# Optimization experiments

Hardware: AMD Instinct MI355X
Metric: run time of the kernel (lower is better)

Reference implementation:

```python
import jax, jax.numpy as jnp
import numpy as np

CHUNK = 128
EPS = 1e-12


def causal_prod(q, k, v, chunk=CHUNK):
    """Chunk-parallel causal linear attention numerator and denominator.
    q,k: [B,H,S,D]; v: [B,H,S,E].
    Returns N: [B,H,S,E] = q_n . cumsum_{m<=n}(k_m v_m^T)
            D: [B,H,S]   = q_n . cumsum_{m<=n} k_m
    """
    B, H, S, D = q.shape
    E = v.shape[-1]
    nc = S // chunk
    # [nc, B, H, C, D]
    qc = q.reshape(B, H, nc, chunk, D).transpose(2, 0, 1, 3, 4)
    kc = k.reshape(B, H, nc, chunk, D).transpose(2, 0, 1, 3, 4)
    vc = v.reshape(B, H, nc, chunk, E).transpose(2, 0, 1, 3, 4)
    mask = jnp.tril(jnp.ones((chunk, chunk), dtype=bool))  # j <= i

    def step(carry, xs):
        S_state, Z_state = carry  # [B,H,D,E], [B,H,D]
        qb, kb, vb = xs           # [B,H,C,D], [B,H,C,D], [B,H,C,E]
        scores = jnp.einsum('bhid,bhjd->bhij', qb, kb)
        scores = jnp.where(mask, scores, 0.0)
        # intra-chunk causal part + inter-chunk state part
        Nb = jnp.einsum('bhij,bhje->bhie', scores, vb) \
             + jnp.einsum('bhid,bhde->bhie', qb, S_state)
        Db = scores.sum(-1) + jnp.einsum('bhid,bhd->bhi', qb, Z_state)
        S_state = S_state + jnp.einsum('bhjd,bhje->bhde', kb, vb)
        Z_state = Z_state + kb.sum(axis=2)
        return (S_state, Z_state), (Nb, Db)

    init = (jnp.zeros((B, H, D, E), q.dtype), jnp.zeros((B, H, D), q.dtype))
    _, (N, Dv) = jax.lax.scan(step, init, (qc, kc, vc))
    N = N.transpose(1, 2, 0, 3, 4).reshape(B, H, S, E)
    Dv = Dv.transpose(1, 2, 0, 3).reshape(B, H, S)
    return N, Dv


def setup_inputs() -> dict:
    key = jax.random.key(0)
    k0, k1, k2, k3, k4 = jax.random.split(key, 5)
    B, H, S, D = 2, 8, 4096, 64
    # feature-mapped q/k are positive (softmax random features) -> uniform
    q = jax.random.uniform(k0, (B, H, S, D), dtype=jnp.float32)
    k = jax.random.uniform(k1, (B, H, S, D), dtype=jnp.float32)
    q_rot = jax.random.uniform(k2, (B, H, S, D), dtype=jnp.float32)
    k_rot = jax.random.uniform(k3, (B, H, S, D), dtype=jnp.float32)
    v = jax.random.normal(k4, (B, H, S, D), dtype=jnp.float32)
    return {"q": q, "k": k, "q_rot": q_rot, "k_rot": k_rot, "v": v, "horizon": 512}


def reference(q, k, q_rot, k_rot, v, horizon):
    # causal_linear_attention with local=horizon, rotary branch active
    N1, D1 = causal_prod(q, k, v)
    N2, D2 = causal_prod(q_rot, k_rot, v)
    N = N1 + N2
    Dd = D1 + D2
    local = horizon
    # subtract contribution of keys older than the local window
    ql = q[:, :, local:]
    kl = k[:, :, :-local]
    vl = v[:, :, :-local]
    qrl = q_rot[:, :, local:]
    krl = k_rot[:, :, :-local]
    Ns1, Ds1 = causal_prod(ql, kl, vl)
    Ns2, Ds2 = causal_prod(qrl, krl, vl)
    N = N.at[:, :, local:].add(-(Ns1 + Ns2))
    Dd = Dd.at[:, :, local:].add(-(Ds1 + Ds2))
    out = N * (1.0 / (Dd + EPS))[..., None]
    return out
```

## Files before the change

### kernel.cpp

```cpp
#include <hip/hip_runtime.h>

#define S_LEN 4096
#define Dh 64

typedef __attribute__((ext_vector_type(8))) short bf16x8;
typedef __attribute__((ext_vector_type(4))) float f32x4;
typedef __attribute__((ext_vector_type(16))) float f32x16;
typedef __attribute__((ext_vector_type(4))) unsigned u32x4;
typedef __attribute__((ext_vector_type(2))) unsigned u32x2;

__device__ __forceinline__ unsigned cvt_pk(float lo, float hi) {
    unsigned r;
    asm("v_cvt_pk_bf16_f32 %0, %1, %2" : "=v"(r) : "v"(lo), "v"(hi));
    return r;
}

__device__ __forceinline__ void pl32swap(unsigned& a, unsigned& b) {
    asm("v_permlane32_swap_b32 %0, %1" : "+v"(a), "+v"(b));
}

__global__ __launch_bounds__(256, 2) void swin_fused(
    const float* __restrict__ q, const float* __restrict__ k,
    const float* __restrict__ qr, const float* __restrict__ kr,
    const float* __restrict__ v, const int* __restrict__ hor,
    float* __restrict__ out)
{
    const int W = hor[0];
    const int nwg = gridDim.x;
    const int cpx = nwg >> 3;
    const int bid = blockIdx.x;
    const int wg = (bid & 7) * cpx + (bid >> 3);
    const int bh = wg >> 5;
    const int q0 = (wg & 31) * 128;
    const size_t base = (size_t)bh * S_LEN * Dh;

    const int tid = threadIdx.x;
    const int lane = tid & 63;
    const int wv = tid >> 6;
    const int hi = lane >> 5;
    const int l32 = lane & 31;

    __shared__ __align__(16) char sK[2][16384];
    __shared__ __align__(16) char sV[2][8192];
    __shared__ float sD[4][32];

    const int q0w = q0 + wv * 32;
    const int qg = q0w + l32;

    bf16x8 qf[8];
    {
        const float* qrow  = q  + base + (size_t)qg * Dh;
        const float* qrrow = qr + base + (size_t)qg * Dh;
        #pragma unroll
        for (int fs = 0; fs < 8; ++fs) {
            int feat = fs * 16 + hi * 8;
            const float* src = (feat < 64) ? (qrow + feat) : (qrrow + feat - 64);
            f32x4 a = *(const f32x4*)src;
            f32x4 b = *(const f32x4*)(src + 4);
            u32x4 w;
            w[0] = cvt_pk(a[0], a[1]); w[1] = cvt_pk(a[2], a[3]);
            w[2] = cvt_pk(b[0], b[1]); w[3] = cvt_pk(b[2], b[3]);
            qf[fs] = __builtin_bit_cast(bf16x8, w);
        }
    }

    f32x16 nacc0 = {};
    f32x16 nacc1 = {};
    float dsum = 0.f;

    const int lo_key = q0 - (W - 1);
    const int kt_lo = (lo_key <= 0) ? 0 : (lo_key >> 6);
    const int kt_hi = (q0 + 127) >> 6;

    f32x4 kfa[4], kfb[4];
    f32x4 vfa[4];

#define LOADT(KT)                                                              \
    do {                                                                       \
        const int k0_ = (KT) << 6;                                             \
        _Pragma("unroll")                                                      \
        for (int i_ = 0; i_ < 4; ++i_) {                                       \
            const int c_ = tid + 256 * i_;                                     \
            const int key_ = c_ >> 4;                                          \
            const int f0_ = (c_ & 15) * 8;                                     \
            const float* s_ = (f0_ < 64)                                       \
                ? (k  + base + (size_t)(k0_ + key_) * Dh + f0_)                \
                : (kr + base + (size_t)(k0_ + key_) * Dh + (f0_ - 64));        \
            kfa[i_] = *(const f32x4*)s_;                                       \
            kfb[i_] = *(const f32x4*)(s_ + 4);                                 \
        }                                                                      \
        _Pragma("unroll")                                                      \
        for (int i_ = 0; i_ < 4; ++i_) {                                       \
            const int c_ = tid + 256 * i_;                                     \
            const int e_ = c_ & 63;                                            \
            const int k4_ = c_ >> 6;                                           \
            const float* s_ = v + base + (size_t)(k0_ + k4_ * 4) * Dh + e_;    \
            f32x4 t_;                                                          \
            t_[0] = s_[0]; t_[1] = s_[Dh]; t_[2] = s_[2 * Dh]; t_[3] = s_[3 * Dh]; \
            vfa[i_] = t_;                                                      \
        }                                                                      \
    } while (0)

#define WRITET(B)                                                              \
    do {                                                                       \
        _Pragma("unroll")                                                      \
        for (int i_ = 0; i_ < 4; ++i_) {                                       \
            const int c_ = tid + 256 * i_;                                     \
            const int key_ = c_ >> 4;                                          \
            const int f0_ = (c_ & 15) * 8;                                     \
            u32x4 w_;                                                          \
            w_[0] = cvt_pk(kfa[i_][0], kfa[i_][1]);                            \
            w_[1] = cvt_pk(kfa[i_][2], kfa[i_][3]);                            \
            w_[2] = cvt_pk(kfb[i_][0], kfb[i_][1]);                            \
            w_[3] = cvt_pk(kfb[i_][2], kfb[i_][3]);                            \
            *(u32x4*)(sK[B] + key_ * 256 + ((f0_ * 2) ^ ((key_ & 15) << 4))) = w_; \
        }                                                                      \
        _Pragma("unroll")                                                      \
        for (int i_ = 0; i_ < 4; ++i_) {                                       \
            const int c_ = tid + 256 * i_;                                     \
            const int e_ = c_ & 63;                                            \
            const int k4_ = c_ >> 6;                                           \
            u32x2 w_;                                                          \
            w_[0] = cvt_pk(vfa[i_][0], vfa[i_][1]);                            \
            w_[1] = cvt_pk(vfa[i_][2], vfa[i_][3]);                            \
            *(u32x2*)(sV[B] + e_ * 128 + ((k4_ * 8) ^ ((e_ & 7) << 4))) = w_;  \
        }                                                                      \
    } while (0)

    LOADT(kt_lo);
    asm volatile("s_waitcnt vmcnt(0)" ::: "memory");
    WRITET(0);
    if (kt_lo < kt_hi) LOADT(kt_lo + 1);
    asm volatile("s_waitcnt lgkmcnt(0)" ::: "memory");
    __builtin_amdgcn_s_barrier();

    int buf = 0;
    for (int kt = kt_lo; kt <= kt_hi; ++kt) {
        const int k0 = kt << 6;

        const bool live = (k0 + 63 >= q0w - W + 1) && (k0 <= q0w + 31);
        if (live) {
            const char* Kb = sK[buf];
            const char* Vb = sV[buf];
            const bool dense = (k0 + 63 <= q0w) && (k0 >= q0w + 32 - W);

            f32x16 sac0 = {};
            f32x16 sac1 = {};
            const int krow = l32 * 256;
            const int ksw = (lane & 15) << 4;
            __builtin_amdgcn_s_setprio(1);
            #pragma unroll
            for (int fs = 0; fs < 8; ++fs) {
                const int fb = (fs * 32 + hi * 16) ^ ksw;
                bf16x8 kf0 = *(const bf16x8*)(Kb + krow + fb);
                bf16x8 kf1 = *(const bf16x8*)(Kb + krow + 8192 + fb);
                sac0 = __builtin_amdgcn_mfma_f32_32x32x16_bf16(kf0, qf[fs], sac0, 0, 0, 0);
                sac1 = __builtin_amdgcn_mfma_f32_32x32x16_bf16(kf1, qf[fs], sac1, 0, 0, 0);
            }
            __builtin_amdgcn_s_setprio(0);

            const int erow = l32 * 128;
            const int esw = (l32 & 7) << 4;
            #pragma unroll
            for (int kb = 0; kb < 2; ++kb) {
                f32x16 s = kb ? sac1 : sac0;
                if (!dense) {
                    #pragma unroll
                    for (int r = 0; r < 16; ++r) {
                        int key = k0 + kb * 32 + (r & 3) + 8 * (r >> 2) + 4 * hi;
                        if ((unsigned)(qg - key) >= (unsigned)W) s[r] = 0.f;
                    }
                }
                #pragma unroll
                for (int r = 0; r < 16; ++r) dsum += s[r];

                unsigned w0 = cvt_pk(s[0],  s[1]);
                unsigned w1 = cvt_pk(s[2],  s[3]);
                unsigned w2 = cvt_pk(s[4],  s[5]);
                unsigned w3 = cvt_pk(s[6],  s[7]);
                unsigned w4 = cvt_pk(s[8],  s[9]);
                unsigned w5 = cvt_pk(s[10], s[11]);
                unsigned w6 = cvt_pk(s[12], s[13]);
                unsigned w7 = cvt_pk(s[14], s[15]);
                pl32swap(w0, w2);
                pl32swap(w1, w3);
                pl32swap(w4, w6);
                pl32swap(w5, w7);
                u32x4 p0v = {w0, w1, w2, w3};
                u32x4 p1v = {w4, w5, w6, w7};
                bf16x8 pa0 = __builtin_bit_cast(bf16x8, p0v);
                bf16x8 pa1 = __builtin_bit_cast(bf16x8, p1v);

                __builtin_amdgcn_s_setprio(1);
                #pragma unroll
                for (int ks = 0; ks < 2; ++ks) {
                    bf16x8 pa = ks ? pa1 : pa0;
                    const int kbyte = ((kb * 32 + ks * 16 + hi * 8) * 2) ^ esw;
                    bf16x8 vf0 = *(const bf16x8*)(Vb + erow + kbyte);
                    bf16x8 vf1 = *(const bf16x8*)(Vb + erow + 4096 + kbyte);
                    nacc0 = __builtin_amdgcn_mfma_f32_32x32x16_bf16(pa, vf0, nacc0, 0, 0, 0);
                    nacc1 = __builtin_amdgcn_mfma_f32_32x32x16_bf16(pa, vf1, nacc1, 0, 0, 0);
                }
                __builtin_amdgcn_s_setprio(0);
            }
        }

        asm volatile("" ::: "memory");
        __builtin_amdgcn_s_barrier();

        if (kt < kt_hi) {
            asm volatile("s_waitcnt vmcnt(0)" ::: "memory");
            WRITET(buf ^ 1);
            if (kt + 1 < kt_hi) LOADT(kt + 2);
            asm volatile("s_waitcnt lgkmcnt(0)" ::: "memory");
            __builtin_amdgcn_s_barrier();
        }
        buf ^= 1;
    }
#undef LOADT
#undef WRITET

    unsigned da = __builtin_bit_cast(unsigned, dsum);
    unsigned db = da;
    pl32swap(da, db);
    float dfull = __builtin_bit_cast(float, da) + __builtin_bit_cast(float, db);
    float rcq = 1.0f / (dfull + 1e-12f);
    if (lane < 32) sD[wv][l32] = rcq;
    __syncthreads();
    float rcv[16];
    #pragma unroll
    for (int r = 0; r < 16; ++r)
        rcv[r] = sD[wv][(r & 3) + 8 * (r >> 2) + 4 * hi];

    #pragma unroll
    for (int r = 0; r < 16; ++r) {
        const int qrow = q0w + (r & 3) + 8 * (r >> 2) + 4 * hi;
        float* o = out + base + (size_t)qrow * Dh + l32;
        o[0]  = nacc0[r] * rcv[r];
        o[32] = nacc1[r] * rcv[r];
    }
}

extern "C" void kernel_launch(void* const* d_in, const int* in_sizes, int n_in,
                              void* d_out, int out_size, void* d_ws, size_t ws_size,
                              hipStream_t stream) {
    const float* q  = (const float*)d_in[0];
    const float* k  = (const float*)d_in[1];
    const float* qr = (const float*)d_in[2];
    const float* kr = (const float*)d_in[3];
    const float* v  = (const float*)d_in[4];
    const int* hor  = (const int*)d_in[5];
    float* out = (float*)d_out;

    const int BH = in_sizes[0] / (S_LEN * Dh);
    hipLaunchKernelGGL(swin_fused, dim3(BH * 32), dim3(256), 0, stream,
                       q, k, qr, kr, v, hor, out);
}
```

Baseline: 42.10 us.

## Deepen K/V prefetch to two register stages and split compute around LDS writes

Global K/V loads now go through two alternating register stage sets, so tiles are prefetched three ahead instead of two, with a partial vmcnt wait. Each iteration computes scores first, then writes the next tile to LDS and issues the next load, and only then runs the PV MFMAs, merging the two barriers per tile into one. The goal is to hide global load latency and cut barrier stalls. The cost is doubled prefetch registers, which may spill at 2 waves/SIMD occupancy, and redundant clamped loads of the final tile at the tail.

```diff
diff --git a/kernel.cpp b/kernel.cpp
--- a/kernel.cpp
+++ b/kernel.cpp
@@ -19,7 +19,7 @@
     asm("v_permlane32_swap_b32 %0, %1" : "+v"(a), "+v"(b));
 }
 
-__global__ __launch_bounds__(256, 2) void swin_fused(
+__global__ __launch_bounds__(256, 2) void swin_fused2(
     const float* __restrict__ q, const float* __restrict__ k,
     const float* __restrict__ qr, const float* __restrict__ kr,
     const float* __restrict__ v, const int* __restrict__ hor,
@@ -72,151 +72,162 @@
     const int kt_lo = (lo_key <= 0) ? 0 : (lo_key >> 6);
     const int kt_hi = (q0 + 127) >> 6;
 
-    f32x4 kfa[4], kfb[4];
-    f32x4 vfa[4];
-
-#define LOADT(KT)                                                              \
-    do {                                                                       \
-        const int k0_ = (KT) << 6;                                             \
-        _Pragma("unroll")                                                      \
-        for (int i_ = 0; i_ < 4; ++i_) {                                       \
-            const int c_ = tid + 256 * i_;                                     \
-            const int key_ = c_ >> 4;                                          \
-            const int f0_ = (c_ & 15) * 8;                                     \
-            const float* s_ = (f0_ < 64)                                       \
-                ? (k  + base + (size_t)(k0_ + key_) * Dh + f0_)                \
-                : (kr + base + (size_t)(k0_ + key_) * Dh + (f0_ - 64));        \
-            kfa[i_] = *(const f32x4*)s_;                                       \
-            kfb[i_] = *(const f32x4*)(s_ + 4);                                 \
-        }                                                                      \
-        _Pragma("unroll")                                                      \
-        for (int i_ = 0; i_ < 4; ++i_) {                                       \
-            const int c_ = tid + 256 * i_;                                     \
-            const int e_ = c_ & 63;                                            \
-            const int k4_ = c_ >> 6;                                           \
-            const float* s_ = v + base + (size_t)(k0_ + k4_ * 4) * Dh + e_;    \
-            f32x4 t_;                                                          \
+    f32x4 kfa_A[4], kfb_A[4], vfa_A[4];
+    f32x4 kfa_B[4], kfb_B[4], vfa_B[4];
+
+#define LOADT(S, KT)                                                            \
+    do {                                                                        \
+        const int k0_ = (KT) << 6;                                              \
+        _Pragma("unroll")                                                       \
+        for (int i_ = 0; i_ < 4; ++i_) {                                        \
+            const int c_ = tid + 256 * i_;                                      \
+            const int key_ = c_ >> 4;                                           \
+            const int f0_ = (c_ & 15) * 8;                                      \
+            const float* s_ = (f0_ < 64)                                        \
+                ? (k  + base + (size_t)(k0_ + key_) * Dh + f0_)                 \
+                : (kr + base + (size_t)(k0_ + key_) * Dh + (f0_ - 64));         \
+            kfa_##S[i_] = *(const f32x4*)s_;                                    \
+            kfb_##S[i_] = *(const f32x4*)(s_ + 4);                              \
+        }                                                                       \
+        _Pragma("unroll")                                                       \
+        for (int i_ = 0; i_ < 4; ++i_) {                                        \
+            const int c_ = tid + 256 * i_;                                      \
+            const int e_ = c_ & 63;                                             \
+            const int k4_ = c_ >> 6;                                            \
+            const float* s_ = v + base + (size_t)(k0_ + k4_ * 4) * Dh + e_;     \
+            f32x4 t_;                                                           \
             t_[0] = s_[0]; t_[1] = s_[Dh]; t_[2] = s_[2 * Dh]; t_[3] = s_[3 * Dh]; \
-            vfa[i_] = t_;                                                      \
-        }                                                                      \
+            vfa_##S[i_] = t_;                                                   \
+        }                                                                       \
     } while (0)
 
-#define WRITET(B)                                                              \
-    do {                                                                       \
-        _Pragma("unroll")                                                      \
-        for (int i_ = 0; i_ < 4; ++i_) {                                       \
-            const int c_ = tid + 256 * i_;                                     \
-            const int key_ = c_ >> 4;                                          \
-            const int f0_ = (c_ & 15) * 8;                                     \
-            u32x4 w_;                                                          \
-            w_[0] = cvt_pk(kfa[i_][0], kfa[i_][1]);                            \
-            w_[1] = cvt_pk(kfa[i_][2], kfa[i_][3]);                            \
-            w_[2] = cvt_pk(kfb[i_][0], kfb[i_][1]);                            \
-            w_[3] = cvt_pk(kfb[i_][2], kfb[i_][3]);                            \
-            *(u32x4*)(sK[B] + key_ * 256 + ((f0_ * 2) ^ ((key_ & 15) << 4))) = w_; \
-        }                                                                      \
-        _Pragma("unroll")                                                      \
-        for (int i_ = 0; i_ < 4; ++i_) {                                       \
-            const int c_ = tid + 256 * i_;                                     \
-            const int e_ = c_ & 63;                                            \
-            const int k4_ = c_ >> 6;                                           \
-            u32x2 w_;                                                          \
-            w_[0] = cvt_pk(vfa[i_][0], vfa[i_][1]);                            \
-            w_[1] = cvt_pk(vfa[i_][2], vfa[i_][3]);                            \
-            *(u32x2*)(sV[B] + e_ * 128 + ((k4_ * 8) ^ ((e_ & 7) << 4))) = w_;  \
-        }                                                                      \
+#define WRITET(B_, S)                                                           \
+    do {                                                                        \
+        _Pragma("unroll")                                                       \
+        for (int i_ = 0; i_ < 4; ++i_) {                                        \
+            const int c_ = tid + 256 * i_;                                      \
+            const int key_ = c_ >> 4;                                           \
+            const int f0_ = (c_ & 15) * 8;                                      \
+            u32x4 w_;                                                           \
+            w_[0] = cvt_pk(kfa_##S[i_][0], kfa_##S[i_][1]);                     \
+            w_[1] = cvt_pk(kfa_##S[i_][2], kfa_##S[i_][3]);                     \
+            w_[2] = cvt_pk(kfb_##S[i_][0], kfb_##S[i_][1]);                     \
+            w_[3] = cvt_pk(kfb_##S[i_][2], kfb_##S[i_][3]);                     \
+            *(u32x4*)(sK[B_] + key_ * 256 + ((f0_ * 2) ^ ((key_ & 15) << 4))) = w_; \
+        }                                                                       \
+        _Pragma("unroll")                                                       \
+        for (int i_ = 0; i_ < 4; ++i_) {                                        \
+            const int c_ = tid + 256 * i_;                                      \
+            const int e_ = c_ & 63;                                             \
+            const int k4_ = c_ >> 6;                                            \
+            u32x2 w_;                                                           \
+            w_[0] = cvt_pk(vfa_##S[i_][0], vfa_##S[i_][1]);                     \
+            w_[1] = cvt_pk(vfa_##S[i_][2], vfa_##S[i_][3]);                     \
+            *(u32x2*)(sV[B_] + e_ * 128 + ((k4_ * 8) ^ ((e_ & 7) << 4))) = w_;  \
+        }                                                                       \
     } while (0)
 
-    LOADT(kt_lo);
     asm volatile("s_waitcnt vmcnt(0)" ::: "memory");
-    WRITET(0);
-    if (kt_lo < kt_hi) LOADT(kt_lo + 1);
+    __builtin_amdgcn_sched_barrier(0);
+    LOADT(A, kt_lo);
+    asm volatile("s_waitcnt vmcnt(0)" ::: "memory");
+    WRITET(0, A);
+    { int t1 = (kt_lo + 1 > kt_hi) ? kt_hi : kt_lo + 1; LOADT(A, t1); }
+    { int t2 = (kt_lo + 2 > kt_hi) ? kt_hi : kt_lo + 2; LOADT(B, t2); }
     asm volatile("s_waitcnt lgkmcnt(0)" ::: "memory");
     __builtin_amdgcn_s_barrier();
 
     int buf = 0;
-    for (int kt = kt_lo; kt <= kt_hi; ++kt) {
-        const int k0 = kt << 6;
-
-        const bool live = (k0 + 63 >= q0w - W + 1) && (k0 <= q0w + 31);
-        if (live) {
-            const char* Kb = sK[buf];
-            const char* Vb = sV[buf];
-            const bool dense = (k0 + 63 <= q0w) && (k0 >= q0w + 32 - W);
-
-            f32x16 sac0 = {};
-            f32x16 sac1 = {};
-            const int krow = l32 * 256;
-            const int ksw = (lane & 15) << 4;
-            __builtin_amdgcn_s_setprio(1);
-            #pragma unroll
-            for (int fs = 0; fs < 8; ++fs) {
-                const int fb = (fs * 32 + hi * 16) ^ ksw;
-                bf16x8 kf0 = *(const bf16x8*)(Kb + krow + fb);
-                bf16x8 kf1 = *(const bf16x8*)(Kb + krow + 8192 + fb);
-                sac0 = __builtin_amdgcn_mfma_f32_32x32x16_bf16(kf0, qf[fs], sac0, 0, 0, 0);
-                sac1 = __builtin_amdgcn_mfma_f32_32x32x16_bf16(kf1, qf[fs], sac1, 0, 0, 0);
-            }
-            __builtin_amdgcn_s_setprio(0);
-
-            const int erow = l32 * 128;
-            const int esw = (l32 & 7) << 4;
-            #pragma unroll
-            for (int kb = 0; kb < 2; ++kb) {
-                f32x16 s = kb ? sac1 : sac0;
-                if (!dense) {
-                    #pragma unroll
-                    for (int r = 0; r < 16; ++r) {
-                        int key = k0 + kb * 32 + (r & 3) + 8 * (r >> 2) + 4 * hi;
-                        if ((unsigned)(qg - key) >= (unsigned)W) s[r] = 0.f;
-                    }
-                }
-                #pragma unroll
-                for (int r = 0; r < 16; ++r) dsum += s[r];
-
-                unsigned w0 = cvt_pk(s[0],  s[1]);
-                unsigned w1 = cvt_pk(s[2],  s[3]);
-                unsigned w2 = cvt_pk(s[4],  s[5]);
-                unsigned w3 = cvt_pk(s[6],  s[7]);
-                unsigned w4 = cvt_pk(s[8],  s[9]);
-                unsigned w5 = cvt_pk(s[10], s[11]);
-                unsigned w6 = cvt_pk(s[12], s[13]);
-                unsigned w7 = cvt_pk(s[14], s[15]);
-                pl32swap(w0, w2);
-                pl32swap(w1, w3);
-                pl32swap(w4, w6);
-                pl32swap(w5, w7);
-                u32x4 p0v = {w0, w1, w2, w3};
-                u32x4 p1v = {w4, w5, w6, w7};
-                bf16x8 pa0 = __builtin_bit_cast(bf16x8, p0v);
-                bf16x8 pa1 = __builtin_bit_cast(bf16x8, p1v);
-
-                __builtin_amdgcn_s_setprio(1);
-                #pragma unroll
-                for (int ks = 0; ks < 2; ++ks) {
-                    bf16x8 pa = ks ? pa1 : pa0;
-                    const int kbyte = ((kb * 32 + ks * 16 + hi * 8) * 2) ^ esw;
-                    bf16x8 vf0 = *(const bf16x8*)(Vb + erow + kbyte);
-                    bf16x8 vf1 = *(const bf16x8*)(Vb + erow + 4096 + kbyte);
-                    nacc0 = __builtin_amdgcn_mfma_f32_32x32x16_bf16(pa, vf0, nacc0, 0, 0, 0);
-                    nacc1 = __builtin_amdgcn_mfma_f32_32x32x16_bf16(pa, vf1, nacc1, 0, 0, 0);
-                }
-                __builtin_amdgcn_s_setprio(0);
-            }
-        }
-
-        asm volatile("" ::: "memory");
-        __builtin_amdgcn_s_barrier();
-
-        if (kt < kt_hi) {
-            asm volatile("s_waitcnt vmcnt(0)" ::: "memory");
-            WRITET(buf ^ 1);
-            if (kt + 1 < kt_hi) LOADT(kt + 2);
-            asm volatile("s_waitcnt lgkmcnt(0)" ::: "memory");
-            __builtin_amdgcn_s_barrier();
-        }
-        buf ^= 1;
+
+#define BODY(KT, S)                                                             \
+    do {                                                                        \
+        const int k0b_ = (KT) << 6;                                             \
+        const bool live_ = (k0b_ + 63 >= q0w - W + 1) && (k0b_ <= q0w + 31);    \
+        const char* Kb_ = sK[buf];                                              \
+        const char* Vb_ = sV[buf];                                              \
+        bf16x8 paA0, paA1, paB0, paB1;                                          \
+        if (live_) {                                                            \
+            const bool dense_ = (k0b_ + 63 <= q0w) && (k0b_ >= q0w + 32 - W);   \
+            f32x16 sac0 = {};                                                   \
+            f32x16 sac1 = {};                                                   \
+            const int ksw_ = (lane & 15) << 4;                                  \
+            const int krow_ = l32 * 256;                                        \
+            __builtin_amdgcn_s_setprio(1);                                      \
+            _Pragma("unroll")                                                   \
+            for (int fs_ = 0; fs_ < 8; ++fs_) {                                 \
+                const int fb_ = (fs_ * 32 + hi * 16) ^ ksw_;                    \
+                bf16x8 kf0 = *(const bf16x8*)(Kb_ + krow_ + fb_);               \
+                bf16x8 kf1 = *(const bf16x8*)(Kb_ + krow_ + 8192 + fb_);        \
+                sac0 = __builtin_amdgcn_mfma_f32_32x32x16_bf16(kf0, qf[fs_], sac0, 0, 0, 0); \
+                sac1 = __builtin_amdgcn_mfma_f32_32x32x16_bf16(kf1, qf[fs_], sac1, 0, 0, 0); \
+            }                                                                   \
+            __builtin_amdgcn_s_setprio(0);                                      \
+            _Pragma("unroll")                                                   \
+            for (int kb_ = 0; kb_ < 2; ++kb_) {                                 \
+                f32x16 s_ = kb_ ? sac1 : sac0;                                  \
+                if (!dense_) {                                                  \
+                    _Pragma("unroll")                                           \
+                    for (int r_ = 0; r_ < 16; ++r_) {                           \
+                        int key_ = k0b_ + kb_ * 32 + (r_ & 3) + 8 * (r_ >> 2) + 4 * hi; \
+                        if ((unsigned)(qg - key_) >= (unsigned)W) s_[r_] = 0.f; \
+                    }                                                           \
+                }                                                               \
+                _Pragma("unroll")                                               \
+                for (int r_ = 0; r_ < 16; ++r_) dsum += s_[r_];                 \
+                unsigned w0_ = cvt_pk(s_[0],  s_[1]);                           \
+                unsigned w1_ = cvt_pk(s_[2],  s_[3]);                           \
+                unsigned w2_ = cvt_pk(s_[4],  s_[5]);                           \
+                unsigned w3_ = cvt_pk(s_[6],  s_[7]);                           \
+                unsigned w4_ = cvt_pk(s_[8],  s_[9]);                           \
+                unsigned w5_ = cvt_pk(s_[10], s_[11]);                          \
+                unsigned w6_ = cvt_pk(s_[12], s_[13]);                          \
+                unsigned w7_ = cvt_pk(s_[14], s_[15]);                          \
+                pl32swap(w0_, w2_);                                             \
+                pl32swap(w1_, w3_);                                             \
+                pl32swap(w4_, w6_);                                             \
+                pl32swap(w5_, w7_);                                             \
+                u32x4 p0v_ = {w0_, w1_, w2_, w3_};                              \
+                u32x4 p1v_ = {w4_, w5_, w6_, w7_};                              \
+                if (kb_ == 0) {                                                 \
+                    paA0 = __builtin_bit_cast(bf16x8, p0v_);                    \
+                    paA1 = __builtin_bit_cast(bf16x8, p1v_);                    \
+                } else {                                                        \
+                    paB0 = __builtin_bit_cast(bf16x8, p0v_);                    \
+                    paB1 = __builtin_bit_cast(bf16x8, p1v_);                    \
+                }                                                               \
+            }                                                                   \
+        }                                                                       \
+        asm volatile("s_waitcnt vmcnt(24)" ::: "memory");   \
+        WRITET(buf ^ 1, S);                                                     \
+        { int nx_ = (KT) + 3; if (nx_ > kt_hi) nx_ = kt_hi; LOADT(S, nx_); }    \
+        if (live_) {                                                            \
+            const int esw_ = (l32 & 7) << 4;                                    \
+            const int erow_ = l32 * 128;                                        \
+            __builtin_amdgcn_s_setprio(1);                                      \
+            _Pragma("unroll")                                                   \
+            for (int kb_ = 0; kb_ < 2; ++kb_) {                                 \
+                _Pragma("unroll")                                               \
+                for (int ks_ = 0; ks_ < 2; ++ks_) {                             \
+                    bf16x8 pa_ = kb_ ? (ks_ ? paB1 : paB0) : (ks_ ? paA1 : paA0); \
+                    const int kbyte_ = ((kb_ * 32 + ks_ * 16 + hi * 8) * 2) ^ esw_; \
+                    bf16x8 vf0 = *(const bf16x8*)(Vb_ + erow_ + kbyte_);        \
+                    bf16x8 vf1 = *(const bf16x8*)(Vb_ + erow_ + 4096 + kbyte_); \
+                    nacc0 = __builtin_amdgcn_mfma_f32_32x32x16_bf16(pa_, vf0, nacc0, 0, 0, 0); \
+                    nacc1 = __builtin_amdgcn_mfma_f32_32x32x16_bf16(pa_, vf1, nacc1, 0, 0, 0); \
+                }                                                               \
+            }                                                                   \
+            __builtin_amdgcn_s_setprio(0);                                      \
+        }                                                                       \
+        asm volatile("s_waitcnt lgkmcnt(0)" ::: "memory");   \
+        __builtin_amdgcn_s_barrier();                                           \
+        buf ^= 1;                                                               \
+    } while (0)
+
+    for (int kt = kt_lo; kt <= kt_hi; kt += 2) {
+        BODY(kt, A);
+        if (kt + 1 <= kt_hi) BODY(kt + 1, B);
     }
+#undef BODY
 #undef LOADT
 #undef WRITET
 
@@ -253,6 +264,6 @@
     float* out = (float*)d_out;
 
     const int BH = in_sizes[0] / (S_LEN * Dh);
-    hipLaunchKernelGGL(swin_fused, dim3(BH * 32), dim3(256), 0, stream,
+    hipLaunchKernelGGL(swin_fused2, dim3(BH * 32), dim3(256), 0, stream,
                        q, k, qr, kr, v, hor, out);
 }
```

After: 55.92 us. 32.8% more time.
